# Kernel optimization log

Hardware: AMD Instinct MI355X
Metric: run time of the kernel (lower is better)

The kernel has to match this reference:

```python
import jax, jax.numpy as jnp
import numpy as np

NEG = -1000.0  # fill value for unmatched (type_mask != ti) entries

B, N, R = 4, 48, 16
T = 2 * R + 1          # 33 transition channels
Nc, L = 80, 3          # chains, chain length
Nt, Ni = 16, 5         # triples, chains per triple (uniform c_sections)


def setup_inputs() -> dict:
    key = jax.random.key(0)
    k1, k2, k3, k4, k5 = jax.random.split(key, 5)
    transitions = jax.random.normal(k1, (B, N, N, T), dtype=jnp.float32)
    type_mask = jax.random.randint(k2, (B, N, N, R), 0, 2, dtype=jnp.int32)
    rules = jax.random.randint(k3, (Nc, L), 0, T, dtype=jnp.int32)
    # stacked per-triple weights [Nt, Ni] (orig: ParameterList of [Ni,1]) and biases [Nt]
    weights = jax.random.normal(k4, (Nt, Ni), dtype=jnp.float32) / np.sqrt(Ni)
    biases = jax.random.uniform(k5, (Nt,), dtype=jnp.float32, minval=-1.0, maxval=1.0)
    return {"transitions": transitions, "type_mask": type_mask, "rules": rules,
            "weights": weights, "biases": biases}


def path_scores(transitions, rules):
    """Tropical (max-plus) chain DP.
    transitions: [B,N,N,T], rules: [Nc,L] -> scores [B,N,N,Nc]
    scores[b,x,y,c] = max over intermediate nodes of sum of hop scores.
    """
    Lc = rules.shape[1]
    hops = [transitions[..., rules[:, l]] for l in range(Lc)]  # each [B,N,N,Nc]
    # max-plus "matmul": s[b,x,y,c] = max_k hops0[b,x,k,c] + hops1[b,k,y,c]
    s = jnp.max(hops[0][:, :, :, None, :] + hops[1][:, None, :, :, :], axis=2)
    for l in range(2, Lc):
        s = jnp.max(s[:, :, :, None, :] + hops[l][:, None, :, :, :], axis=2)
    return s


def reference(transitions, type_mask, rules, weights, biases):
    # scores over all chains, exponentiated: [B,N,N,Nc]
    s = jnp.exp(path_scores(transitions, rules))
    # group chains by triple (uniform sections): [B,N,N,Nt,Ni]
    s = s.reshape(s.shape[0], s.shape[1], s.shape[2], Nt, Ni)
    # per-triple weighted sum + bias; one triple per relation so Nt == R
    comb = jnp.einsum('bxytc,tc->bxyt', s, weights) + biases  # [B,N,N,R]
    # masked_scatter: write score where type_mask[...,i] == ti (== 0 here), else -1000
    out = jnp.where(type_mask == 0, comb, NEG)
    return out
```

## Files before the change

### kernel.cpp

```cpp
#include <hip/hip_runtime.h>
#include <cmath>

#define BB 4
#define NN 48
#define TT 33
#define RR 16
#define NC 80
#define NI 5
#define NEG (-1000.0f)

#define XS 24
#define XP 25
#define NTH 192
#define NTILE 96

__global__ __launch_bounds__(NTH) void chain_dp_kernel(
    const float* __restrict__ trans,
    const int*   __restrict__ rules,
    const float* __restrict__ weights,
    float*       __restrict__ sw)
{
    __shared__ float H0T[NN * XP];
    __shared__ float H1 [NN * NN];
    __shared__ float H2 [NN * NN];
    __shared__ float S1T[NN * XP];
    __shared__ float Pa [NN * XP];

    const int blk = blockIdx.x;
    const int bc  = blk >> 1;
    const int xh  = blk & 1;
    const int b   = bc / NC;
    const int c   = bc - b * NC;
    const int xbase = xh * XS;

    const int r0 = rules[c * 3 + 0];
    const int r1 = rules[c * 3 + 1];
    const int r2 = rules[c * 3 + 2];

    const float* tb = trans + (size_t)b * NN * NN * TT;

    for (int i = threadIdx.x; i < XS * NN; i += NTH) {
        const int xl = i / NN;
        const int k  = i - xl * NN;
        H0T[k * XP + xl] = tb[(size_t)((xbase + xl) * NN + k) * TT + r0];
    }
    for (int i = threadIdx.x; i < NN * NN; i += NTH) {
        const size_t base = (size_t)i * TT;
        H1[i] = tb[base + r1];
        H2[i] = tb[base + r2];
    }
    __syncthreads();

    const int g  = threadIdx.x / NTILE;
    const int w  = threadIdx.x - g * NTILE;
    const int tx = w & 7;
    const int ty = w >> 3;
    const int x0 = tx * 3;
    const int y0 = ty * 4;
    const int k0 = g * 24;

    float acc[3][4];
    #pragma unroll
    for (int jx = 0; jx < 3; ++jx)
        #pragma unroll
        for (int jy = 0; jy < 4; ++jy) acc[jx][jy] = -INFINITY;

    #pragma unroll 4
    for (int kp = 0; kp < 12; ++kp) {
        const int k = k0 + kp * 2;
        float a0[3], a1[3];
        #pragma unroll
        for (int jx = 0; jx < 3; ++jx) {
            a0[jx] = H0T[k * XP + x0 + jx];
            a1[jx] = H0T[(k + 1) * XP + x0 + jx];
        }
        const float4 bv0 = *(const float4*)&H1[k * NN + y0];
        const float4 bv1 = *(const float4*)&H1[(k + 1) * NN + y0];
        const float b0[4] = {bv0.x, bv0.y, bv0.z, bv0.w};
        const float b1[4] = {bv1.x, bv1.y, bv1.z, bv1.w};
        #pragma unroll
        for (int jx = 0; jx < 3; ++jx)
            #pragma unroll
            for (int jy = 0; jy < 4; ++jy)
                acc[jx][jy] = fmaxf(acc[jx][jy],
                                    fmaxf(a0[jx] + b0[jy], a1[jx] + b1[jy]));
    }

    {
        float* dst = (g == 0) ? S1T : Pa;
        #pragma unroll
        for (int jx = 0; jx < 3; ++jx)
            #pragma unroll
            for (int jy = 0; jy < 4; ++jy)
                dst[(y0 + jy) * XP + x0 + jx] = acc[jx][jy];
    }
    __syncthreads();

    for (int j = threadIdx.x; j < NN * XP; j += NTH)
        S1T[j] = fmaxf(S1T[j], Pa[j]);
    __syncthreads();

    float acc2[3][4];
    #pragma unroll
    for (int jx = 0; jx < 3; ++jx)
        #pragma unroll
        for (int jy = 0; jy < 4; ++jy) acc2[jx][jy] = -INFINITY;

    #pragma unroll 4
    for (int kp = 0; kp < 12; ++kp) {
        const int k = k0 + kp * 2;
        float a0[3], a1[3];
        #pragma unroll
        for (int jx = 0; jx < 3; ++jx) {
            a0[jx] = S1T[k * XP + x0 + jx];
            a1[jx] = S1T[(k + 1) * XP + x0 + jx];
        }
        const float4 bv0 = *(const float4*)&H2[k * NN + y0];
        const float4 bv1 = *(const float4*)&H2[(k + 1) * NN + y0];
        const float b0[4] = {bv0.x, bv0.y, bv0.z, bv0.w};
        const float b1[4] = {bv1.x, bv1.y, bv1.z, bv1.w};
        #pragma unroll
        for (int jx = 0; jx < 3; ++jx)
            #pragma unroll
            for (int jy = 0; jy < 4; ++jy)
                acc2[jx][jy] = fmaxf(acc2[jx][jy],
                                     fmaxf(a0[jx] + b0[jy], a1[jx] + b1[jy]));
    }

    if (g == 1) {
        #pragma unroll
        for (int jx = 0; jx < 3; ++jx)
            #pragma unroll
            for (int jy = 0; jy < 4; ++jy)
                Pa[(jx * 4 + jy) * NTILE + w] = acc2[jx][jy];
    }
    __syncthreads();

    if (g == 0) {
        const float wgt = weights[c];
        float* outp = sw + (size_t)bc * NN * NN;
        #pragma unroll
        for (int jx = 0; jx < 3; ++jx)
            #pragma unroll
            for (int jy = 0; jy < 4; ++jy) {
                const float m = fmaxf(acc2[jx][jy], Pa[(jx * 4 + jy) * NTILE + w]);
                outp[(xbase + x0 + jx) * NN + y0 + jy] = __expf(m) * wgt;
            }
    }
}

__global__ __launch_bounds__(256) void combine_kernel(
    const float* __restrict__ sw,
    const int*   __restrict__ mask,
    const float* __restrict__ biases,
    float*       __restrict__ out)
{
    const int tq = threadIdx.x >> 7;
    const int pl = blockIdx.x * 128 + (threadIdx.x & 127);
    if (pl >= BB * NN * NN) return;
    const int b = pl / (NN * NN);
    const int p = pl - b * (NN * NN);

    const float* base = sw + (size_t)b * NC * NN * NN + p;

    float acc[8];
    #pragma unroll
    for (int tt = 0; tt < 8; ++tt) {
        const int t = tq * 8 + tt;
        float s = biases[t];
        #pragma unroll
        for (int i = 0; i < NI; ++i)
            s += base[(size_t)(t * NI + i) * NN * NN];
        acc[tt] = s;
    }

    const int4* m4 = (const int4*)(mask + (size_t)pl * RR + tq * 8);
    float4*     o4 = (float4*)(out + (size_t)pl * RR + tq * 8);
    #pragma unroll
    for (int q = 0; q < 2; ++q) {
        const int4 m = m4[q];
        float4 o;
        o.x = (m.x == 0) ? acc[q * 4 + 0] : NEG;
        o.y = (m.y == 0) ? acc[q * 4 + 1] : NEG;
        o.z = (m.z == 0) ? acc[q * 4 + 2] : NEG;
        o.w = (m.w == 0) ? acc[q * 4 + 3] : NEG;
        o4[q] = o;
    }
}

extern "C" void kernel_launch(void* const* d_in, const int* in_sizes, int n_in,
                              void* d_out, int out_size, void* d_ws, size_t ws_size,
                              hipStream_t stream)
{
    const float* trans   = (const float*)d_in[0];
    const int*   mask    = (const int*)  d_in[1];
    const int*   rules   = (const int*)  d_in[2];
    const float* weights = (const float*)d_in[3];
    const float* biases  = (const float*)d_in[4];
    float* out = (float*)d_out;
    float* sw  = (float*)d_ws;

    chain_dp_kernel<<<BB * NC * 2, NTH, 0, stream>>>(trans, rules, weights, sw);

    const int total2 = BB * NN * NN * 2;
    combine_kernel<<<(total2 + 255) / 256, 256, 0, stream>>>(sw, mask, biases, out);
}
```

Measured before the change: 78.99 us.

## Pre-transpose transitions to channel-major and use one block per chain

Adds a transpose kernel that rewrites transitions into [B,T,N*N] layout so the chain DP kernel can load each hop plane with coalesced float4 reads instead of strided gathers at stride 33. The DP kernel now processes the full 48x48 tile per block with 192 threads, dropping the k-split partial reductions and their extra LDS buffer and syncs, and writes outputs as float4. This costs an extra kernel launch and a global round trip of the transition tensor, and halves the number of DP blocks, which lowers parallelism across the GPU.

```diff
diff --git a/kernel.cpp b/kernel.cpp
--- a/kernel.cpp
+++ b/kernel.cpp
@@ -3,61 +3,75 @@
 
 #define BB 4
 #define NN 48
+#define PP (NN * NN)
+#define NP 49
 #define TT 33
 #define RR 16
 #define NC 80
 #define NI 5
 #define NEG (-1000.0f)
 
-#define XS 24
-#define XP 25
-#define NTH 192
-#define NTILE 96
-
-__global__ __launch_bounds__(NTH) void chain_dp_kernel(
+__global__ __launch_bounds__(256) void transpose_kernel(
     const float* __restrict__ trans,
+    float*       __restrict__ tpose)
+{
+    __shared__ float tile[64 * TT];
+    const int blk = blockIdx.x;
+    const int b   = blk / 36;
+    const int p0  = (blk - b * 36) * 64;
+
+    const float4* src = (const float4*)(trans + ((size_t)b * PP + p0) * TT);
+    for (int j = threadIdx.x; j < 64 * TT / 4; j += 256)
+        ((float4*)tile)[j] = src[j];
+    __syncthreads();
+
+    for (int j = threadIdx.x; j < TT * 64; j += 256) {
+        const int t  = j >> 6;
+        const int pl = j & 63;
+        tpose[((size_t)b * TT + t) * PP + p0 + pl] = tile[pl * TT + t];
+    }
+}
+
+__global__ __launch_bounds__(192) void chain_dp_kernel(
+    const float* __restrict__ tpose,
     const int*   __restrict__ rules,
     const float* __restrict__ weights,
     float*       __restrict__ sw)
 {
-    __shared__ float H0T[NN * XP];
-    __shared__ float H1 [NN * NN];
-    __shared__ float H2 [NN * NN];
-    __shared__ float S1T[NN * XP];
-    __shared__ float Pa [NN * XP];
-
-    const int blk = blockIdx.x;
-    const int bc  = blk >> 1;
-    const int xh  = blk & 1;
-    const int b   = bc / NC;
-    const int c   = bc - b * NC;
-    const int xbase = xh * XS;
+    __shared__ float H0T[NN * NP];
+    __shared__ float H1 [PP];
+    __shared__ float H2 [PP];
+    __shared__ float S1T[NN * NP];
+
+    const int bc = blockIdx.x;
+    const int b  = bc / NC;
+    const int c  = bc - b * NC;
 
     const int r0 = rules[c * 3 + 0];
     const int r1 = rules[c * 3 + 1];
     const int r2 = rules[c * 3 + 2];
 
-    const float* tb = trans + (size_t)b * NN * NN * TT;
-
-    for (int i = threadIdx.x; i < XS * NN; i += NTH) {
-        const int xl = i / NN;
-        const int k  = i - xl * NN;
-        H0T[k * XP + xl] = tb[(size_t)((xbase + xl) * NN + k) * TT + r0];
-    }
-    for (int i = threadIdx.x; i < NN * NN; i += NTH) {
-        const size_t base = (size_t)i * TT;
-        H1[i] = tb[base + r1];
-        H2[i] = tb[base + r2];
+    const float* p0 = tpose + ((size_t)b * TT + r0) * PP;
+    const float* p1 = tpose + ((size_t)b * TT + r1) * PP;
+    const float* p2 = tpose + ((size_t)b * TT + r2) * PP;
+
+    for (int j = threadIdx.x; j < PP / 4; j += 192) {
+        ((float4*)H1)[j] = ((const float4*)p1)[j];
+        ((float4*)H2)[j] = ((const float4*)p2)[j];
+        const float4 v0 = ((const float4*)p0)[j];
+        const int x = (4 * j) / NN;
+        const int k = (4 * j) - x * NN;
+        H0T[(k + 0) * NP + x] = v0.x;
+        H0T[(k + 1) * NP + x] = v0.y;
+        H0T[(k + 2) * NP + x] = v0.z;
+        H0T[(k + 3) * NP + x] = v0.w;
     }
     __syncthreads();
 
-    const int g  = threadIdx.x / NTILE;
-    const int w  = threadIdx.x - g * NTILE;
-    const int tx = w & 7;
-    const int ty = w >> 3;
+    const int tx = threadIdx.x & 15;
+    const int ty = threadIdx.x >> 4;
     const int x0 = tx * 3;
     const int y0 = ty * 4;
-    const int k0 = g * 24;
 
     float acc[3][4];
     #pragma unroll
@@ -66,13 +80,13 @@
         for (int jy = 0; jy < 4; ++jy) acc[jx][jy] = -INFINITY;
 
     #pragma unroll 4
-    for (int kp = 0; kp < 12; ++kp) {
-        const int k = k0 + kp * 2;
+    for (int kp = 0; kp < NN / 2; ++kp) {
+        const int k = kp * 2;
         float a0[3], a1[3];
         #pragma unroll
         for (int jx = 0; jx < 3; ++jx) {
-            a0[jx] = H0T[k * XP + x0 + jx];
-            a1[jx] = H0T[(k + 1) * XP + x0 + jx];
+            a0[jx] = H0T[k * NP + x0 + jx];
+            a1[jx] = H0T[(k + 1) * NP + x0 + jx];
         }
         const float4 bv0 = *(const float4*)&H1[k * NN + y0];
         const float4 bv1 = *(const float4*)&H1[(k + 1) * NN + y0];
@@ -86,20 +100,13 @@
                                     fmaxf(a0[jx] + b0[jy], a1[jx] + b1[jy]));
     }
 
-    {
-        float* dst = (g == 0) ? S1T : Pa;
-        #pragma unroll
-        for (int jx = 0; jx < 3; ++jx)
-            #pragma unroll
-            for (int jy = 0; jy < 4; ++jy)
-                dst[(y0 + jy) * XP + x0 + jx] = acc[jx][jy];
-    }
+    #pragma unroll
+    for (int jx = 0; jx < 3; ++jx)
+        #pragma unroll
+        for (int jy = 0; jy < 4; ++jy)
+            S1T[(y0 + jy) * NP + x0 + jx] = acc[jx][jy];
     __syncthreads();
 
-    for (int j = threadIdx.x; j < NN * XP; j += NTH)
-        S1T[j] = fmaxf(S1T[j], Pa[j]);
-    __syncthreads();
-
     float acc2[3][4];
     #pragma unroll
     for (int jx = 0; jx < 3; ++jx)
@@ -107,13 +114,13 @@
         for (int jy = 0; jy < 4; ++jy) acc2[jx][jy] = -INFINITY;
 
     #pragma unroll 4
-    for (int kp = 0; kp < 12; ++kp) {
-        const int k = k0 + kp * 2;
+    for (int kp = 0; kp < NN / 2; ++kp) {
+        const int k = kp * 2;
         float a0[3], a1[3];
         #pragma unroll
         for (int jx = 0; jx < 3; ++jx) {
-            a0[jx] = S1T[k * XP + x0 + jx];
-            a1[jx] = S1T[(k + 1) * XP + x0 + jx];
+            a0[jx] = S1T[k * NP + x0 + jx];
+            a1[jx] = S1T[(k + 1) * NP + x0 + jx];
         }
         const float4 bv0 = *(const float4*)&H2[k * NN + y0];
         const float4 bv1 = *(const float4*)&H2[(k + 1) * NN + y0];
@@ -127,25 +134,16 @@
                                      fmaxf(a0[jx] + b0[jy], a1[jx] + b1[jy]));
     }
 
-    if (g == 1) {
-        #pragma unroll
-        for (int jx = 0; jx < 3; ++jx)
-            #pragma unroll
-            for (int jy = 0; jy < 4; ++jy)
-                Pa[(jx * 4 + jy) * NTILE + w] = acc2[jx][jy];
-    }
-    __syncthreads();
-
-    if (g == 0) {
-        const float wgt = weights[c];
-        float* outp = sw + (size_t)bc * NN * NN;
-        #pragma unroll
-        for (int jx = 0; jx < 3; ++jx)
-            #pragma unroll
-            for (int jy = 0; jy < 4; ++jy) {
-                const float m = fmaxf(acc2[jx][jy], Pa[(jx * 4 + jy) * NTILE + w]);
-                outp[(xbase + x0 + jx) * NN + y0 + jy] = __expf(m) * wgt;
-            }
+    const float wgt = weights[c];
+    float* outp = sw + (size_t)bc * PP;
+    #pragma unroll
+    for (int jx = 0; jx < 3; ++jx) {
+        float4 o;
+        o.x = __expf(acc2[jx][0]) * wgt;
+        o.y = __expf(acc2[jx][1]) * wgt;
+        o.z = __expf(acc2[jx][2]) * wgt;
+        o.w = __expf(acc2[jx][3]) * wgt;
+        *(float4*)&outp[(x0 + jx) * NN + y0] = o;
     }
 }
 
@@ -157,11 +155,11 @@
 {
     const int tq = threadIdx.x >> 7;
     const int pl = blockIdx.x * 128 + (threadIdx.x & 127);
-    if (pl >= BB * NN * NN) return;
-    const int b = pl / (NN * NN);
-    const int p = pl - b * (NN * NN);
-
-    const float* base = sw + (size_t)b * NC * NN * NN + p;
+    if (pl >= BB * PP) return;
+    const int b = pl / PP;
+    const int p = pl - b * PP;
+
+    const float* base = sw + (size_t)b * NC * PP + p;
 
     float acc[8];
     #pragma unroll
@@ -170,7 +168,7 @@
         float s = biases[t];
         #pragma unroll
         for (int i = 0; i < NI; ++i)
-            s += base[(size_t)(t * NI + i) * NN * NN];
+            s += base[(size_t)(t * NI + i) * PP];
         acc[tt] = s;
     }
 
@@ -198,10 +196,14 @@
     const float* weights = (const float*)d_in[3];
     const float* biases  = (const float*)d_in[4];
     float* out = (float*)d_out;
-    float* sw  = (float*)d_ws;
-
-    chain_dp_kernel<<<BB * NC * 2, NTH, 0, stream>>>(trans, rules, weights, sw);
-
-    const int total2 = BB * NN * NN * 2;
+
+    float* tpose = (float*)d_ws;
+    float* sw    = tpose + (size_t)BB * TT * PP;
+
+    transpose_kernel<<<BB * 36, 256, 0, stream>>>(trans, tpose);
+
+    chain_dp_kernel<<<BB * NC, 192, 0, stream>>>(tpose, rules, weights, sw);
+
+    const int total2 = BB * PP * 2;
     combine_kernel<<<(total2 + 255) / 256, 256, 0, stream>>>(sw, mask, biases, out);
 }
```

New measurement: 75.23 us. 4.8% less time.
